# Performance work log

Hardware: AMD Instinct MI355X
Metric: run time of the kernel (lower is better)

The kernel has to match this reference:

```python
import jax, jax.numpy as jnp
import numpy as np

N_QUBITS = 14
DEPTH = 8
NUM_BLOCKS = DEPTH // 2
BATCH = 256
INIT_SCALE = 0.1


def _ry_mat(theta):
    # RY(t) = [[cos(t/2), -sin(t/2)], [sin(t/2), cos(t/2)]]; works for scalar or batched theta
    c = jnp.cos(theta / 2).astype(jnp.complex64)
    s = jnp.sin(theta / 2).astype(jnp.complex64)
    return jnp.stack([jnp.stack([c, -s], -1), jnp.stack([s, c], -1)], -2)


def _rz_mat(theta):
    # RZ(t) = diag(exp(-i t/2), exp(+i t/2))
    e = jnp.exp(-0.5j * theta.astype(jnp.complex64))
    z = jnp.zeros_like(e)
    return jnp.stack([jnp.stack([e, z], -1), jnp.stack([z, jnp.conj(e)], -1)], -2)


def _rx_mat(theta):
    # RX(t) = [[cos(t/2), -i sin(t/2)], [-i sin(t/2), cos(t/2)]] (target block of CRX)
    c = jnp.cos(theta / 2).astype(jnp.complex64)
    s = (-1j) * jnp.sin(theta / 2).astype(jnp.complex64)
    return jnp.stack([jnp.stack([c, s], -1), jnp.stack([s, c], -1)], -2)


def _apply_1q(state, mat, q, n):
    # state: (B, 2**n) complex64. Wire 0 = most significant axis (PennyLane convention).
    B = state.shape[0]
    s = state.reshape(B, 2 ** q, 2, 2 ** (n - q - 1))
    if mat.ndim == 3:  # per-sample angles (input encoding layer)
        out = jnp.einsum('bij,bljr->blir', mat, s)
    else:
        out = jnp.einsum('ij,bljr->blir', mat, s)
    return out.reshape(B, -1)


def _apply_ctrl(state, mat, c, t, n):
    # Apply 2x2 `mat` on target wire t where control wire c == 1.
    B = state.shape[0]
    s = state.reshape(B, 2 ** c, 2, 2 ** (n - c - 1))
    sub = s[:, :, 1, :]  # control = |1> subspace, (B, 2**c, 2**(n-c-1))
    p = t if t < c else t - 1  # target position in the reduced (n-1)-qubit register
    sub2 = sub.reshape(B, 2 ** p, 2, 2 ** (n - 2 - p))
    sub2 = jnp.einsum('ij,bljr->blir', mat, sub2)
    return s.at[:, :, 1, :].set(sub2.reshape(sub.shape)).reshape(B, -1)


def _circuit(inputs, weights):
    n, nb = N_QUBITS, NUM_BLOCKS
    B = inputs.shape[0]
    state = jnp.zeros((B, 2 ** n), jnp.complex64).at[:, 0].set(1.0)
    # input encoding: RY(inputs[..., q]) on each wire (batched angles)
    for q in range(n):
        state = _apply_1q(state, _ry_mat(inputs[:, q]), q, n)
    # weights flat index = b*3n + layer*n + q  ->  reshape (nb, 3, n)
    w = weights.reshape(nb, 3, n)
    X = jnp.asarray([[0, 1], [1, 0]], dtype=jnp.complex64)

    def block(st, wb):
        for q in range(n):
            st = _apply_1q(st, _ry_mat(wb[0, q]), q, n)
        for q in range(n):
            st = _apply_ctrl(st, X, q, (q + 1) % n, n)  # CNOT ring
        for q in range(n):
            st = _apply_1q(st, _rz_mat(wb[1, q]), q, n)
        for q in range(n):
            st = _apply_ctrl(st, _rx_mat(wb[2, q]), q, (q + 1) % n, n)  # CRX ring
        return st

    block = jax.checkpoint(block)
    for b in range(nb):
        state = block(state, w[b])

    # <Z_q> = P(bit_q = 0) - P(bit_q = 1)
    probs = state.real ** 2 + state.imag ** 2
    outs = []
    for q in range(n):
        pq = probs.reshape(B, 2 ** q, 2, -1)
        outs.append(pq[:, :, 0, :].sum((1, 2)) - pq[:, :, 1, :].sum((1, 2)))
    return jnp.stack(outs, -1).astype(jnp.float32)


def setup_inputs() -> dict:
    key = jax.random.key(0)
    k1, k2 = jax.random.split(key)
    inputs = jax.random.normal(k1, (BATCH, N_QUBITS), dtype=jnp.float32)
    weights = INIT_SCALE * jax.random.normal(k2, (3 * N_QUBITS * NUM_BLOCKS,), dtype=jnp.float32)
    return {"inputs": inputs, "weights": weights}


def reference(inputs, weights):
    return _circuit(inputs, weights)
```

## Files before the change

kernel.cpp:

```cpp
#include <hip/hip_runtime.h>
#include <utility>

#define NQ 14
#define NST (1 << NQ)
#define THREADS 1024

typedef float f2 __attribute__((ext_vector_type(2)));

struct PassD {
    unsigned short comboR[16];
    unsigned short rows[4];
    unsigned short tmask[4];
    unsigned short crx_widx[3];
    unsigned short ry_widx[3];
    unsigned char  ry_tb[3];
    unsigned char  ncrx;
    unsigned char  nry;
    short          rzidx;
    unsigned char  measfold;
};
struct RZD  { unsigned short rows_ng[10]; unsigned short widx_ng[10]; unsigned short widx_g[4]; };
struct AllD { PassD pass[20]; RZD rz[4]; unsigned short meas_rows_ng[10]; int npass; };

constexpr void fill_geom(PassD& P, const unsigned short* R, const unsigned short* C, const int* tb)
{
    for (int i = 0; i < 4; ++i) { P.tmask[i] = C[tb[i]]; P.rows[i] = R[tb[i]]; }
    for (int j = 0; j < 16; ++j) {
        unsigned short x = 0;
        for (int i = 0; i < 4; ++i) if ((j >> i) & 1) x = (unsigned short)(x ^ P.tmask[i]);
        P.comboR[j] = x;
    }
}

constexpr void ring(unsigned short* R, unsigned short* C) {
    for (int q = 0; q < NQ; ++q) {
        int cb = 13 - q, tb = 13 - ((q + 1) % NQ);
        R[tb] = (unsigned short)(R[tb] ^ R[cb]);
        C[cb] = (unsigned short)(C[cb] ^ C[tb]);
    }
}

constexpr AllD build_desc() {
    AllD A{};
    unsigned short R[NQ] = {}, C[NQ] = {};
    for (int k = 0; k < NQ; ++k) { R[k] = (unsigned short)(1u << k); C[k] = (unsigned short)(1u << k); }
    int np = 0;
    const int tiles[5][4] = {{13,12,11,10},{10,9,8,7},{7,6,5,4},{4,3,2,1},{1,0,13,2}};
    const int gfirst[5]   = {0, 3, 6, 9, 12};
    const int ngate[5]    = {3, 3, 3, 3, 2};
    const int rybits[5][3]= {{11,12,0},{10,9,8},{7,6,5},{4,3,2},{13,1,0}};
    const int nryp[5]     = {2, 3, 3, 3, 3};

    for (int blk = 0; blk < 4; ++blk) {
        ring(R, C);
        for (int pi = 0; pi < 5; ++pi) {
            PassD& P = A.pass[np];
            fill_geom(P, R, C, tiles[pi]);
            P.ncrx = (unsigned char)ngate[pi];
            for (int g = 0; g < 3; ++g)
                P.crx_widx[g] = (unsigned short)((g < ngate[pi]) ? blk*42 + 28 + gfirst[pi] + g : 0);
            if (blk < 3) {
                P.nry = (unsigned char)nryp[pi];
                for (int g = 0; g < 3; ++g) {
                    if (g < nryp[pi]) {
                        int k = rybits[pi][g];
                        P.ry_widx[g] = (unsigned short)((blk + 1)*42 + (13 - k));
                        int t = 0;
                        for (int i = 0; i < 4; ++i) if (tiles[pi][i] == k) t = i;
                        P.ry_tb[g] = (unsigned char)t;
                    } else { P.ry_widx[g] = 0; P.ry_tb[g] = 0; }
                }
            } else { P.nry = 0; for (int g = 0; g < 3; ++g) { P.ry_widx[g] = 0; P.ry_tb[g] = 0; } }
            P.rzidx = (short)((pi == 0) ? blk : -1);
            P.measfold = (unsigned char)((blk == 3 && pi == 4) ? 1 : 0);
            if (pi == 0) {
                RZD& Z = A.rz[blk];
                for (int i = 0; i < 4; ++i)
                    Z.widx_g[i] = (unsigned short)(blk*42 + 14 + (13 - tiles[0][i]));
                int t = 0;
                for (int q = 4; q < NQ; ++q, ++t) {
                    Z.rows_ng[t] = R[13 - q];
                    Z.widx_ng[t] = (unsigned short)(blk*42 + 14 + q);
                }
            }
            ++np;
        }
        if (blk == 3)
            for (int t = 0; t < 10; ++t) A.meas_rows_ng[t] = R[13 - (1 + t)];
    }
    A.npass = np;
    return A;
}

constexpr AllD A = build_desc();
static_assert(A.npass == 20, "expected 20 passes");

constexpr int parity14(unsigned v) { v ^= v >> 8; v ^= v >> 4; v ^= v >> 2; v ^= v >> 1; return (int)(v & 1); }

constexpr bool check_dual() {
    for (int p = 0; p < 20; ++p)
        for (int i = 0; i < 4; ++i)
            for (int j = 0; j < 4; ++j)
                if (parity14((unsigned)(A.pass[p].rows[i] & A.pass[p].tmask[j])) != (i == j ? 1 : 0))
                    return false;
    return true;
}
static_assert(check_dual(), "R/C duality violated");

struct GWT { unsigned short w[20][6]; };
constexpr GWT build_gwt() {
    GWT g{};
    for (int p = 0; p < 20; ++p) {
        for (int s = 0; s < 3; ++s) g.w[p][s]     = A.pass[p].crx_widx[s];
        for (int s = 0; s < 3; ++s) g.w[p][3 + s] = A.pass[p].ry_widx[s];
    }
    return g;
}
constexpr GWT GW = build_gwt();

constexpr int lead(unsigned short v) { int b = 13; while (b > 0 && !((v >> b) & 1)) --b; return b; }

struct Span {
    unsigned short red[14]; int n;
    constexpr unsigned short reduce(unsigned short v) const {
        for (int i = 0; i < n; ++i) { int lb = lead(red[i]); if ((v >> lb) & 1) v = (unsigned short)(v ^ red[i]); }
        return v;
    }
    constexpr bool add(unsigned short v) {
        unsigned short r = reduce(v);
        if (!r) return false;
        red[n++] = r; return true;
    }
};

constexpr unsigned short proj(unsigned short vec, const PassD& P) {
    unsigned short r = vec;
    for (int t = 0; t < 4; ++t)
        if (parity14((unsigned)(vec & P.rows[t]))) r = (unsigned short)(r ^ P.tmask[t]);
    return r;
}

struct VecsT { unsigned short lane[20][6]; unsigned short g[10][4]; int ok; };
constexpr VecsT build_vecs() {
    VecsT V{}; V.ok = 1;
    for (int k = 0; k < 10; ++k) {
        const PassD& P0 = A.pass[2*k];
        const PassD& P1 = A.pass[2*k + 1];
        Span SW{}; unsigned short Wb[10] = {}; int nw = 0;
        for (int i = 0; i < 4; ++i) if (SW.add(P0.tmask[i])) Wb[nw++] = P0.tmask[i];
        for (int i = 0; i < 4; ++i) if (nw < 10 && SW.add(P1.tmask[i])) Wb[nw++] = P1.tmask[i];
        for (int b = 0; b < 14 && nw < 10; ++b) {
            unsigned short e = (unsigned short)(1u << b);
            if (SW.add(e)) Wb[nw++] = e;
        }
        if (nw != 10) V.ok = 0;
        Span SG = SW; int ngv = 0;
        for (int b = 0; b < 14 && ngv < 4; ++b) {
            unsigned short e = (unsigned short)(1u << b);
            if (SG.add(e)) V.g[k][ngv++] = e;
        }
        if (ngv != 4) V.ok = 0;
        for (int pp = 0; pp < 2; ++pp) {
            const PassD& P = (pp == 0) ? P0 : P1;
            int pidx = 2*k + pp;
            Span ST{};
            for (int i = 0; i < 4; ++i) ST.add(P.tmask[i]);
            int nl = 0;
            for (int i = 0; i < 10 && nl < 6; ++i)
                if (ST.add(Wb[i])) V.lane[pidx][nl++] = Wb[i];
            if (nl != 6) V.ok = 0;
            Span SF{};
            for (int i = 0; i < 4; ++i) SF.add(P.tmask[i]);
            for (int i = 0; i < 6; ++i) if (!SF.add(V.lane[pidx][i])) V.ok = 0;
            for (int i = 0; i < 4; ++i) if (!SF.add(V.g[k][i])) V.ok = 0;
            if (SF.n != 14) V.ok = 0;
        }
    }
    return V;
}
constexpr VecsT VC = build_vecs();
static_assert(VC.ok == 1, "vec construction failed");

struct P6T { unsigned short u[20][6]; };
constexpr P6T build_p6() {
    P6T X{};
    for (int p = 0; p < 20; ++p)
        for (int i = 0; i < 6; ++i)
            X.u[p][i] = proj(VC.lane[p][i], A.pass[p]);
    return X;
}
constexpr P6T P6 = build_p6();

constexpr unsigned lmap(const unsigned short* row, unsigned x) {
    unsigned l = 0;
    for (int t = 0; t < 4; ++t) l |= (unsigned)parity14(row[t] & x) << t;
    return l;
}
constexpr int nib_rank(const unsigned* nibs, int n) {
    unsigned basis[4] = {};
    int r = 0;
    for (int i = 0; i < n; ++i) {
        unsigned v = nibs[i] & 15u;
        for (int b = 3; b >= 0 && v; --b) {
            if (!((v >> b) & 1)) continue;
            if (basis[b]) v ^= basis[b];
            else { basis[b] = v; ++r; v = 0; }
        }
    }
    return r;
}
struct Lp { unsigned short row[4]; int score; };

constexpr int full_score(const unsigned short* r) {
    unsigned cn[4] = {};
    for (int c = 0; c < 4; ++c) {
        unsigned v = 0;
        for (int t = 0; t < 4; ++t) v |= ((unsigned)(r[t] >> c) & 1u) << t;
        cn[c] = v;
    }
    if (nib_rank(cn, 4) != 4) return -1;
    int sc = 0;
    for (int p = 0; p < 20; ++p) {
        unsigned im[6] = {};
        for (int i = 0; i < 6; ++i) im[i] = lmap(r, P6.u[p][i]);
        if (nib_rank(im, 6) == 4) ++sc;
    }
    return sc;
}

constexpr Lp search_stage(unsigned seed, int iters) {
    Lp best{}; best.score = -1;
    unsigned s = seed;
    for (int it = 0; it < iters; ++it) {
        unsigned short r[4] = {};
        for (int t = 0; t < 4; ++t) { s = s*1664525u + 1013904223u; r[t] = (unsigned short)((s >> 9) & 0x3FFF); }
        unsigned cn[4] = {};
        for (int c = 0; c < 4; ++c) {
            unsigned v = 0;
            for (int t = 0; t < 4; ++t) v |= ((unsigned)(r[t] >> c) & 1u) << t;
            cn[c] = v;
        }
        if (nib_rank(cn, 4) != 4) continue;
        int sc = 0;
        for (int p = 0; p < 20; ++p) {
            unsigned im[6] = {};
            for (int i = 0; i < 6; ++i) im[i] = lmap(r, P6.u[p][i]);
            if (nib_rank(im, 6) != 4) break;
            ++sc;
        }
        if (sc > best.score) { best.score = sc; for (int t = 0; t < 4; ++t) best.row[t] = r[t]; }
        if (best.score == 20) break;
    }
    return best;
}
constexpr Lp S0 = search_stage(0x12345u, 500);
constexpr Lp S1 = search_stage(0xBEEF1u, 500);
constexpr Lp S2 = search_stage(0xC0FFEu, 500);
constexpr Lp S3 = search_stage(0x777A1u, 500);
constexpr Lp S4 = search_stage(0x51DE5u, 500);
constexpr Lp S5 = search_stage(0xA11CEu, 500);
constexpr Lp S6 = search_stage(0x0F00Du, 500);
constexpr Lp S7 = search_stage(0x9E3779u & 0xFFFFF, 500);
constexpr Lp S8 = search_stage(0x13579u, 500);
constexpr Lp S9 = search_stage(0x2468Au, 500);
constexpr Lp S10 = search_stage(0xFACE1u, 500);
constexpr Lp S11 = search_stage(0xD00D1u, 500);
constexpr Lp pick_best() {
    Lp b = S0;
    if (S1.score  > b.score) b = S1;
    if (S2.score  > b.score) b = S2;
    if (S3.score  > b.score) b = S3;
    if (S4.score  > b.score) b = S4;
    if (S5.score  > b.score) b = S5;
    if (S6.score  > b.score) b = S6;
    if (S7.score  > b.score) b = S7;
    if (S8.score  > b.score) b = S8;
    if (S9.score  > b.score) b = S9;
    if (S10.score > b.score) b = S10;
    if (S11.score > b.score) b = S11;
    return b;
}
constexpr Lp climb(Lp start, int sweeps) {
    Lp cur = start;
    for (int sw = 0; sw < sweeps && cur.score < 20; ++sw) {
        for (int t = 0; t < 4; ++t) {
            for (int b = 0; b < 14; ++b) {
                if (cur.score >= 20) break;
                unsigned short nr[4] = {cur.row[0], cur.row[1], cur.row[2], cur.row[3]};
                nr[t] = (unsigned short)(nr[t] ^ (1u << b));
                int sc = full_score(nr);
                if (sc > cur.score) { cur.score = sc; cur.row[t] = nr[t]; }
            }
        }
    }
    return cur;
}
constexpr Lp C0 = climb(pick_best(), 2);
constexpr Lp C1 = climb(C0, 2);
constexpr Lp LSEL = C1;
static_assert(LSEL.score >= 17, "bank-map search regressed");

constexpr unsigned short swz2(unsigned short x) {
    return (unsigned short)(((unsigned)x & ~15u) | lmap(LSEL.row, x));
}

constexpr int add_basis4(unsigned* basis, unsigned v) {
    for (int b = 3; b >= 0; --b) {
        if (!((v >> b) & 1)) continue;
        if (basis[b]) v ^= basis[b];
        else { basis[b] = v; return 1; }
    }
    return 0;
}
constexpr int add_basis6(unsigned* basis, unsigned v) {
    for (int b = 5; b >= 0; --b) {
        if (!((v >> b) & 1)) continue;
        if (basis[b]) v ^= basis[b];
        else { basis[b] = v; return 1; }
    }
    return 0;
}
struct LaneOrd { unsigned short lane[20][6]; };
constexpr LaneOrd build_lane2() {
    LaneOrd O{};
    for (int p = 0; p < 20; ++p) {
        for (int i = 0; i < 6; ++i) O.lane[p][i] = VC.lane[p][i];
        unsigned imu[6] = {};
        for (int i = 0; i < 6; ++i) imu[i] = lmap(LSEL.row, P6.u[p][i]);
        {
            unsigned chk[6] = {imu[0], imu[1], imu[2], imu[3], imu[4], imu[5]};
            if (nib_rank(chk, 6) != 4) continue;
        }
        unsigned short nl[6] = {};
        int ns = 0;
        unsigned ib[4] = {};
        unsigned sb[6] = {};
        for (unsigned c = 1; c < 64 && ns < 4; ++c) {
            unsigned img = 0; unsigned short rv = 0;
            for (int i = 0; i < 6; ++i) if ((c >> i) & 1) { img ^= imu[i]; rv = (unsigned short)(rv ^ VC.lane[p][i]); }
            if (img == 0) continue;
            unsigned ib2[4] = {ib[0], ib[1], ib[2], ib[3]};
            unsigned sb2[6] = {sb[0], sb[1], sb[2], sb[3], sb[4], sb[5]};
            if (add_basis4(ib2, img) && add_basis6(sb2, c)) {
                for (int t = 0; t < 4; ++t) ib[t] = ib2[t];
                for (int t = 0; t < 6; ++t) sb[t] = sb2[t];
                nl[ns++] = rv;
            }
        }
        for (unsigned c = 1; c < 64 && ns < 6; ++c) {
            unsigned img = 0; unsigned short rv = 0;
            for (int i = 0; i < 6; ++i) if ((c >> i) & 1) { img ^= imu[i]; rv = (unsigned short)(rv ^ VC.lane[p][i]); }
            if (img != 0) continue;
            unsigned sb2[6] = {sb[0], sb[1], sb[2], sb[3], sb[4], sb[5]};
            if (add_basis6(sb2, c)) {
                for (int t = 0; t < 6; ++t) sb[t] = sb2[t];
                nl[ns++] = rv;
            }
        }
        if (ns == 6)
            for (int i = 0; i < 6; ++i) O.lane[p][i] = nl[i];
    }
    return O;
}
constexpr LaneOrd LO = build_lane2();

struct CS2 { unsigned short c[20][16]; };
constexpr CS2 build_cs2() {
    CS2 C{};
    for (int p = 0; p < 20; ++p)
        for (int j = 0; j < 16; ++j)
            C.c[p][j] = swz2(A.pass[p].comboR[j]);
    return C;
}
constexpr CS2 CSS = build_cs2();

struct LJt { unsigned short v[16]; };
constexpr LJt build_lj() {
    LJt t{};
    for (int j = 0; j < 16; ++j) t.v[j] = (unsigned short)lmap(LSEL.row, (unsigned)(j * 1024));
    return t;
}
constexpr LJt LJ = build_lj();

constexpr unsigned pack_entry(unsigned short vec0, int p) {
    const PassD& P = A.pass[p];
    unsigned short vec = proj(vec0, P);
    unsigned par = 0;
    if (P.rzidx >= 0)
        for (int t = 0; t < 10; ++t) par |= (unsigned)parity14(vec & A.rz[P.rzidx].rows_ng[t]) << t;
    if (P.measfold)
        for (int t = 0; t < 10; ++t) par |= (unsigned)parity14(vec & A.meas_rows_ng[t]) << t;
    return ((unsigned)swz2(vec) << 3) | (par << 22);
}

struct LutsT { unsigned v[20][2][32]; };
constexpr LutsT build_luts() {
    LutsT L{};
    for (int p = 0; p < 20; ++p) {
        int k = p >> 1;
        for (int t = 0; t < 32; ++t) {
            unsigned short x = 0;
            for (int i = 0; i < 5; ++i) if ((t >> i) & 1) x = (unsigned short)(x ^ LO.lane[p][i]);
            L.v[p][0][t] = pack_entry(x, p);
            unsigned short y = 0;
            if (t & 1) y = (unsigned short)(y ^ LO.lane[p][5]);
            for (int i = 0; i < 4; ++i) if ((t >> (i + 1)) & 1) y = (unsigned short)(y ^ VC.g[k][i]);
            L.v[p][1][t] = pack_entry(y, p);
        }
    }
    return L;
}
constexpr LutsT LUTS = build_luts();
__device__ __constant__ LutsT cLUTS = LUTS;

template<int Pi>
__device__ __forceinline__ void run_pass(f2* st, const f2 (*tabG)[6], const float (*tabRZ)[14],
                                         unsigned comb, float* acc)
{
    constexpr PassD Pd = A.pass[Pi];
    char* stb = (char*)st;
    const int base = (int)(comb & 0x1FFF8u);
    const unsigned par = comb >> 22;

    f2 v[16];
#pragma unroll
    for (int j = 0; j < 16; ++j)
        v[j] = *(const f2*)(stb + (base ^ (CSS.c[Pi][j] << 3)));

    if constexpr (Pd.rzidx >= 0) {
        float phi0 = 0.f;
#pragma unroll
        for (int t = 0; t < 10; ++t) {
            float h = tabRZ[Pd.rzidx][t];
            phi0 += ((par >> t) & 1) ? h : -h;
        }
        const float h0 = tabRZ[Pd.rzidx][10], h1 = tabRZ[Pd.rzidx][11];
        const float h2 = tabRZ[Pd.rzidx][12], h3 = tabRZ[Pd.rzidx][13];
#pragma unroll
        for (int j = 0; j < 16; ++j) {
            float phi = ((((phi0 + ((j & 1) ? h0 : -h0)) + ((j & 2) ? h1 : -h1))
                                 + ((j & 4) ? h2 : -h2)) + ((j & 8) ? h3 : -h3));
            float s, c; __sincosf(phi, &s, &c);
            f2 C = {c, c}, S = {-s, s};
            v[j] = C * v[j] + S * v[j].yx;
        }
    }

#pragma unroll
    for (int g = 0; g < Pd.ncrx; ++g) {
        f2 cs = tabG[Pi][g];
        f2 C = {cs.x, cs.x}, S = {cs.y, -cs.y};
#pragma unroll
        for (int j = 0; j < 16; ++j) if (((j >> g) & 1) && !((j >> (g + 1)) & 1)) {
            int j1 = j | (1 << (g + 1));
            f2 a0 = v[j], a1 = v[j1];
            v[j]  = C * a0 + S * a1.yx;
            v[j1] = C * a1 + S * a0.yx;
        }
    }

#pragma unroll
    for (int g = 0; g < Pd.nry; ++g) {
        int t = Pd.ry_tb[g];
        f2 cs = tabG[Pi][3 + g];
        f2 C = {cs.x, cs.x}, Sv = {cs.y, cs.y}, NS = {-cs.y, -cs.y};
#pragma unroll
        for (int j = 0; j < 16; ++j) if (!((j >> t) & 1)) {
            int j1 = j | (1 << t);
            f2 a0 = v[j], a1 = v[j1];
            v[j]  = C * a0 + NS * a1;
            v[j1] = Sv * a0 + C * a1;
        }
    }

    if constexpr (Pd.measfold != 0) {
        f2 ps = {0.f, 0.f}, p0 = {0.f, 0.f}, p1 = {0.f, 0.f}, p2 = {0.f, 0.f}, p3 = {0.f, 0.f};
#pragma unroll
        for (int j = 0; j < 16; ++j) {
            f2 t2 = v[j] * v[j];
            ps += t2;
            if (j & 1) p0 += t2;
            if (j & 2) p1 += t2;
            if (j & 4) p2 += t2;
            if (j & 8) p3 += t2;
        }
        float psum = ps.x + ps.y;
        float pg0 = p0.x + p0.y, pg1 = p1.x + p1.y, pg2 = p2.x + p2.y, pg3 = p3.x + p3.y;
        acc[12] += psum - 2.f * pg0;
        acc[13] += psum - 2.f * pg1;
        acc[0]  += psum - 2.f * pg2;
        acc[11] += psum - 2.f * pg3;
#pragma unroll
        for (int t = 0; t < 10; ++t) {
            float sg = ((par >> t) & 1) ? -1.f : 1.f;
            acc[1 + t] += sg * psum;
        }
    } else {
#pragma unroll
        for (int j = 0; j < 16; ++j)
            *(f2*)(stb + (base ^ (CSS.c[Pi][j] << 3))) = v[j];
        if constexpr ((Pi & 1) != 0) __syncthreads();
    }
}

template<int... I>
__device__ __forceinline__ void run_all(std::integer_sequence<int, I...>,
                                        f2* st, const f2 (*tabG)[6], const float (*tabRZ)[14],
                                        const unsigned* comb, float* acc)
{
    (run_pass<I>(st, tabG, tabRZ, comb[I], acc), ...);
}

__global__ __launch_bounds__(THREADS, 4)
void qsim_kernel(const float* __restrict__ inputs,
                 const float* __restrict__ weights,
                 float* __restrict__ out)
{
    __shared__ f2     st[NST];
    __shared__ float  tab[256];
    __shared__ f2     tabG[20][6];
    __shared__ float  tabRZ[4][14];
    __shared__ float  red[THREADS / 64][NQ];

    const int b = blockIdx.x;
    const int tid = threadIdx.x;

    unsigned comb[20];
#pragma unroll
    for (int p = 0; p < 20; ++p)
        comb[p] = cLUTS.v[p][0][tid & 31] ^ cLUTS.v[p][1][tid >> 5];

    if (tid < 120) {
        int p = tid / 6, sl = tid - p * 6;
        float w = weights[GW.w[p][sl]];
        float s, c; __sincosf(0.5f * w, &s, &c);
        tabG[p][sl] = (f2){c, s};
    } else if (tid >= 128 && tid < 128 + 56) {
        int idx = tid - 128;
        int blk = idx / 14, k = idx - blk * 14;
        unsigned wi = (k < 10) ? A.rz[blk].widx_ng[k] : A.rz[blk].widx_g[k - 10];
        tabRZ[blk][k] = 0.5f * weights[wi];
    } else if (tid >= 256 && tid < 512) {
        int t = tid - 256;
        int half = t >> 7, tt = t & 127;
        float prod = 1.f;
#pragma unroll
        for (int j = 0; j < 7; ++j) {
            int xb = j + 7 * half;
            int q  = 13 - xb;
            float a = 0.5f * (inputs[b * NQ + q] + weights[q]);
            float s, c; __sincosf(a, &s, &c);
            prod *= ((tt >> j) & 1) ? s : c;
        }
        tab[t] = prod;
    }
    __syncthreads();

    unsigned l4t = 0;
#pragma unroll
    for (int t = 0; t < 4; ++t)
        l4t |= (unsigned)(__popc((int)(LSEL.row[t] & tid)) & 1) << t;
#pragma unroll
    for (int j = 0; j < 16; ++j) {
        int x = tid + j * THREADS;
        int addr = (x & ~15) | (int)(l4t ^ LJ.v[j]);
        st[addr] = (f2){tab[x & 127] * tab[128 + (x >> 7)], 0.f};
    }
    __syncthreads();

    float acc[NQ];
#pragma unroll
    for (int q = 0; q < NQ; ++q) acc[q] = 0.f;

    run_all(std::make_integer_sequence<int, 20>{}, st, tabG, tabRZ, comb, acc);

#pragma unroll
    for (int q = 0; q < NQ; ++q) {
        float v2 = acc[q];
        v2 += __shfl_down(v2, 32);
        v2 += __shfl_down(v2, 16);
        v2 += __shfl_down(v2, 8);
        v2 += __shfl_down(v2, 4);
        v2 += __shfl_down(v2, 2);
        v2 += __shfl_down(v2, 1);
        acc[q] = v2;
    }
    const int wave = tid >> 6, lane = tid & 63;
    if (lane == 0) {
#pragma unroll
        for (int q = 0; q < NQ; ++q) red[wave][q] = acc[q];
    }
    __syncthreads();
    if (tid < NQ) {
        float v2 = 0.f;
#pragma unroll
        for (int w = 0; w < THREADS / 64; ++w) v2 += red[w][tid];
        out[b * NQ + tid] = v2;
    }
}

extern "C" void kernel_launch(void* const* d_in, const int* in_sizes, int n_in,
                              void* d_out, int out_size, void* d_ws, size_t ws_size,
                              hipStream_t stream) {
    const float* inputs  = (const float*)d_in[0];
    const float* weights = (const float*)d_in[1];
    float* out = (float*)d_out;
    const int B = in_sizes[0] / NQ;
    qsim_kernel<<<dim3(B), dim3(THREADS), 0, stream>>>(inputs, weights, out);
}
```

Baseline: 46.47 us.

## Use 5-qubit tiles with 512 threads to cut passes from 20 to 16

Enlarges each register-resident tile from 4 to 5 qubits, so each thread holds 32 amplitudes instead of 16. The block shrinks to 512 threads and the gate schedule is regrouped into 4 passes per block instead of 5. This cuts shared-memory round trips and barriers. The costs are higher register pressure, lower occupancy per block, and a weaker bank-conflict map score (the assert is relaxed to at least 13 of 16 passes), so there may be more LDS bank conflicts.

```diff
diff --git a/kernel.cpp b/kernel.cpp
--- a/kernel.cpp
+++ b/kernel.cpp
@@ -3,31 +3,33 @@
 
 #define NQ 14
 #define NST (1 << NQ)
-#define THREADS 1024
+#define THREADS 512
+#define NP 16
+#define NE 32
 
 typedef float f2 __attribute__((ext_vector_type(2)));
 
 struct PassD {
-    unsigned short comboR[16];
-    unsigned short rows[4];
-    unsigned short tmask[4];
-    unsigned short crx_widx[3];
-    unsigned short ry_widx[3];
-    unsigned char  ry_tb[3];
+    unsigned short comboR[NE];
+    unsigned short rows[5];
+    unsigned short tmask[5];
+    unsigned short crx_widx[4];
+    unsigned short ry_widx[4];
+    unsigned char  ry_tb[4];
     unsigned char  ncrx;
     unsigned char  nry;
     short          rzidx;
     unsigned char  measfold;
 };
-struct RZD  { unsigned short rows_ng[10]; unsigned short widx_ng[10]; unsigned short widx_g[4]; };
-struct AllD { PassD pass[20]; RZD rz[4]; unsigned short meas_rows_ng[10]; int npass; };
+struct RZD  { unsigned short rows_ng[9]; unsigned short widx_ng[9]; unsigned short widx_g[5]; };
+struct AllD { PassD pass[NP]; RZD rz[4]; unsigned short meas_rows_ng[9]; int npass; };
 
 constexpr void fill_geom(PassD& P, const unsigned short* R, const unsigned short* C, const int* tb)
 {
-    for (int i = 0; i < 4; ++i) { P.tmask[i] = C[tb[i]]; P.rows[i] = R[tb[i]]; }
-    for (int j = 0; j < 16; ++j) {
+    for (int i = 0; i < 5; ++i) { P.tmask[i] = C[tb[i]]; P.rows[i] = R[tb[i]]; }
+    for (int j = 0; j < NE; ++j) {
         unsigned short x = 0;
-        for (int i = 0; i < 4; ++i) if ((j >> i) & 1) x = (unsigned short)(x ^ P.tmask[i]);
+        for (int i = 0; i < 5; ++i) if ((j >> i) & 1) x = (unsigned short)(x ^ P.tmask[i]);
         P.comboR[j] = x;
     }
 }
@@ -45,40 +47,40 @@
     unsigned short R[NQ] = {}, C[NQ] = {};
     for (int k = 0; k < NQ; ++k) { R[k] = (unsigned short)(1u << k); C[k] = (unsigned short)(1u << k); }
     int np = 0;
-    const int tiles[5][4] = {{13,12,11,10},{10,9,8,7},{7,6,5,4},{4,3,2,1},{1,0,13,2}};
-    const int gfirst[5]   = {0, 3, 6, 9, 12};
-    const int ngate[5]    = {3, 3, 3, 3, 2};
-    const int rybits[5][3]= {{11,12,0},{10,9,8},{7,6,5},{4,3,2},{13,1,0}};
-    const int nryp[5]     = {2, 3, 3, 3, 3};
+    const int tiles[4][5]  = {{13,12,11,10,9},{9,8,7,6,5},{5,4,3,2,1},{1,0,13,3,2}};
+    const int gfirst[4]    = {0, 4, 8, 12};
+    const int ngate[4]     = {4, 4, 4, 2};
+    const int rybits[4][4] = {{12,11,10,0},{9,8,7,6},{5,4,3,2},{13,1,0,0}};
+    const int nryp[4]      = {3, 4, 4, 3};
 
     for (int blk = 0; blk < 4; ++blk) {
         ring(R, C);
-        for (int pi = 0; pi < 5; ++pi) {
+        for (int pi = 0; pi < 4; ++pi) {
             PassD& P = A.pass[np];
             fill_geom(P, R, C, tiles[pi]);
             P.ncrx = (unsigned char)ngate[pi];
-            for (int g = 0; g < 3; ++g)
+            for (int g = 0; g < 4; ++g)
                 P.crx_widx[g] = (unsigned short)((g < ngate[pi]) ? blk*42 + 28 + gfirst[pi] + g : 0);
             if (blk < 3) {
                 P.nry = (unsigned char)nryp[pi];
-                for (int g = 0; g < 3; ++g) {
+                for (int g = 0; g < 4; ++g) {
                     if (g < nryp[pi]) {
                         int k = rybits[pi][g];
                         P.ry_widx[g] = (unsigned short)((blk + 1)*42 + (13 - k));
                         int t = 0;
-                        for (int i = 0; i < 4; ++i) if (tiles[pi][i] == k) t = i;
+                        for (int i = 0; i < 5; ++i) if (tiles[pi][i] == k) t = i;
                         P.ry_tb[g] = (unsigned char)t;
                     } else { P.ry_widx[g] = 0; P.ry_tb[g] = 0; }
                 }
-            } else { P.nry = 0; for (int g = 0; g < 3; ++g) { P.ry_widx[g] = 0; P.ry_tb[g] = 0; } }
+            } else { P.nry = 0; for (int g = 0; g < 4; ++g) { P.ry_widx[g] = 0; P.ry_tb[g] = 0; } }
             P.rzidx = (short)((pi == 0) ? blk : -1);
-            P.measfold = (unsigned char)((blk == 3 && pi == 4) ? 1 : 0);
+            P.measfold = (unsigned char)((blk == 3 && pi == 3) ? 1 : 0);
             if (pi == 0) {
                 RZD& Z = A.rz[blk];
-                for (int i = 0; i < 4; ++i)
+                for (int i = 0; i < 5; ++i)
                     Z.widx_g[i] = (unsigned short)(blk*42 + 14 + (13 - tiles[0][i]));
                 int t = 0;
-                for (int q = 4; q < NQ; ++q, ++t) {
+                for (int q = 5; q < NQ; ++q, ++t) {
                     Z.rows_ng[t] = R[13 - q];
                     Z.widx_ng[t] = (unsigned short)(blk*42 + 14 + q);
                 }
@@ -86,33 +88,33 @@
             ++np;
         }
         if (blk == 3)
-            for (int t = 0; t < 10; ++t) A.meas_rows_ng[t] = R[13 - (1 + t)];
+            for (int t = 0; t < 9; ++t) A.meas_rows_ng[t] = R[13 - (1 + t)];
     }
     A.npass = np;
     return A;
 }
 
 constexpr AllD A = build_desc();
-static_assert(A.npass == 20, "expected 20 passes");
+static_assert(A.npass == NP, "expected 16 passes");
 
 constexpr int parity14(unsigned v) { v ^= v >> 8; v ^= v >> 4; v ^= v >> 2; v ^= v >> 1; return (int)(v & 1); }
 
 constexpr bool check_dual() {
-    for (int p = 0; p < 20; ++p)
-        for (int i = 0; i < 4; ++i)
-            for (int j = 0; j < 4; ++j)
+    for (int p = 0; p < NP; ++p)
+        for (int i = 0; i < 5; ++i)
+            for (int j = 0; j < 5; ++j)
                 if (parity14((unsigned)(A.pass[p].rows[i] & A.pass[p].tmask[j])) != (i == j ? 1 : 0))
                     return false;
     return true;
 }
 static_assert(check_dual(), "R/C duality violated");
 
-struct GWT { unsigned short w[20][6]; };
+struct GWT { unsigned short w[NP][8]; };
 constexpr GWT build_gwt() {
     GWT g{};
-    for (int p = 0; p < 20; ++p) {
-        for (int s = 0; s < 3; ++s) g.w[p][s]     = A.pass[p].crx_widx[s];
-        for (int s = 0; s < 3; ++s) g.w[p][3 + s] = A.pass[p].ry_widx[s];
+    for (int p = 0; p < NP; ++p) {
+        for (int s = 0; s < 4; ++s) g.w[p][s]     = A.pass[p].crx_widx[s];
+        for (int s = 0; s < 4; ++s) g.w[p][4 + s] = A.pass[p].ry_widx[s];
     }
     return g;
 }
@@ -135,44 +137,44 @@
 
 constexpr unsigned short proj(unsigned short vec, const PassD& P) {
     unsigned short r = vec;
-    for (int t = 0; t < 4; ++t)
+    for (int t = 0; t < 5; ++t)
         if (parity14((unsigned)(vec & P.rows[t]))) r = (unsigned short)(r ^ P.tmask[t]);
     return r;
 }
 
-struct VecsT { unsigned short lane[20][6]; unsigned short g[10][4]; int ok; };
+struct VecsT { unsigned short lane[NP][6]; unsigned short g[NP/2][3]; int ok; };
 constexpr VecsT build_vecs() {
     VecsT V{}; V.ok = 1;
-    for (int k = 0; k < 10; ++k) {
+    for (int k = 0; k < NP/2; ++k) {
         const PassD& P0 = A.pass[2*k];
         const PassD& P1 = A.pass[2*k + 1];
-        Span SW{}; unsigned short Wb[10] = {}; int nw = 0;
-        for (int i = 0; i < 4; ++i) if (SW.add(P0.tmask[i])) Wb[nw++] = P0.tmask[i];
-        for (int i = 0; i < 4; ++i) if (nw < 10 && SW.add(P1.tmask[i])) Wb[nw++] = P1.tmask[i];
-        for (int b = 0; b < 14 && nw < 10; ++b) {
+        Span SW{}; unsigned short Wb[11] = {}; int nw = 0;
+        for (int i = 0; i < 5; ++i) if (SW.add(P0.tmask[i])) Wb[nw++] = P0.tmask[i];
+        for (int i = 0; i < 5; ++i) if (nw < 11 && SW.add(P1.tmask[i])) Wb[nw++] = P1.tmask[i];
+        for (int b = 0; b < 14 && nw < 11; ++b) {
             unsigned short e = (unsigned short)(1u << b);
             if (SW.add(e)) Wb[nw++] = e;
         }
-        if (nw != 10) V.ok = 0;
+        if (nw != 11) V.ok = 0;
         Span SG = SW; int ngv = 0;
-        for (int b = 0; b < 14 && ngv < 4; ++b) {
+        for (int b = 0; b < 14 && ngv < 3; ++b) {
             unsigned short e = (unsigned short)(1u << b);
             if (SG.add(e)) V.g[k][ngv++] = e;
         }
-        if (ngv != 4) V.ok = 0;
+        if (ngv != 3) V.ok = 0;
         for (int pp = 0; pp < 2; ++pp) {
             const PassD& P = (pp == 0) ? P0 : P1;
             int pidx = 2*k + pp;
             Span ST{};
-            for (int i = 0; i < 4; ++i) ST.add(P.tmask[i]);
+            for (int i = 0; i < 5; ++i) ST.add(P.tmask[i]);
             int nl = 0;
-            for (int i = 0; i < 10 && nl < 6; ++i)
+            for (int i = 0; i < 11 && nl < 6; ++i)
                 if (ST.add(Wb[i])) V.lane[pidx][nl++] = Wb[i];
             if (nl != 6) V.ok = 0;
             Span SF{};
-            for (int i = 0; i < 4; ++i) SF.add(P.tmask[i]);
+            for (int i = 0; i < 5; ++i) SF.add(P.tmask[i]);
             for (int i = 0; i < 6; ++i) if (!SF.add(V.lane[pidx][i])) V.ok = 0;
-            for (int i = 0; i < 4; ++i) if (!SF.add(V.g[k][i])) V.ok = 0;
+            for (int i = 0; i < 3; ++i) if (!SF.add(V.g[k][i])) V.ok = 0;
             if (SF.n != 14) V.ok = 0;
         }
     }
@@ -181,10 +183,10 @@
 constexpr VecsT VC = build_vecs();
 static_assert(VC.ok == 1, "vec construction failed");
 
-struct P6T { unsigned short u[20][6]; };
+struct P6T { unsigned short u[NP][6]; };
 constexpr P6T build_p6() {
     P6T X{};
-    for (int p = 0; p < 20; ++p)
+    for (int p = 0; p < NP; ++p)
         for (int i = 0; i < 6; ++i)
             X.u[p][i] = proj(VC.lane[p][i], A.pass[p]);
     return X;
@@ -220,7 +222,7 @@
     }
     if (nib_rank(cn, 4) != 4) return -1;
     int sc = 0;
-    for (int p = 0; p < 20; ++p) {
+    for (int p = 0; p < NP; ++p) {
         unsigned im[6] = {};
         for (int i = 0; i < 6; ++i) im[i] = lmap(r, P6.u[p][i]);
         if (nib_rank(im, 6) == 4) ++sc;
@@ -234,58 +236,37 @@
     for (int it = 0; it < iters; ++it) {
         unsigned short r[4] = {};
         for (int t = 0; t < 4; ++t) { s = s*1664525u + 1013904223u; r[t] = (unsigned short)((s >> 9) & 0x3FFF); }
-        unsigned cn[4] = {};
-        for (int c = 0; c < 4; ++c) {
-            unsigned v = 0;
-            for (int t = 0; t < 4; ++t) v |= ((unsigned)(r[t] >> c) & 1u) << t;
-            cn[c] = v;
-        }
-        if (nib_rank(cn, 4) != 4) continue;
-        int sc = 0;
-        for (int p = 0; p < 20; ++p) {
-            unsigned im[6] = {};
-            for (int i = 0; i < 6; ++i) im[i] = lmap(r, P6.u[p][i]);
-            if (nib_rank(im, 6) != 4) break;
-            ++sc;
-        }
+        int sc = full_score(r);
         if (sc > best.score) { best.score = sc; for (int t = 0; t < 4; ++t) best.row[t] = r[t]; }
-        if (best.score == 20) break;
+        if (best.score == NP) break;
     }
     return best;
 }
-constexpr Lp S0 = search_stage(0x12345u, 500);
-constexpr Lp S1 = search_stage(0xBEEF1u, 500);
-constexpr Lp S2 = search_stage(0xC0FFEu, 500);
-constexpr Lp S3 = search_stage(0x777A1u, 500);
-constexpr Lp S4 = search_stage(0x51DE5u, 500);
-constexpr Lp S5 = search_stage(0xA11CEu, 500);
-constexpr Lp S6 = search_stage(0x0F00Du, 500);
-constexpr Lp S7 = search_stage(0x9E3779u & 0xFFFFF, 500);
-constexpr Lp S8 = search_stage(0x13579u, 500);
-constexpr Lp S9 = search_stage(0x2468Au, 500);
-constexpr Lp S10 = search_stage(0xFACE1u, 500);
-constexpr Lp S11 = search_stage(0xD00D1u, 500);
+constexpr Lp S0 = search_stage(0x12345u, 400);
+constexpr Lp S1 = search_stage(0xBEEF1u, 400);
+constexpr Lp S2 = search_stage(0xC0FFEu, 400);
+constexpr Lp S3 = search_stage(0x777A1u, 400);
+constexpr Lp S4 = search_stage(0x51DE5u, 400);
+constexpr Lp S5 = search_stage(0xA11CEu, 400);
+constexpr Lp S6 = search_stage(0x0F00Du, 400);
+constexpr Lp S7 = search_stage(0x13579u, 400);
 constexpr Lp pick_best() {
     Lp b = S0;
-    if (S1.score  > b.score) b = S1;
-    if (S2.score  > b.score) b = S2;
-    if (S3.score  > b.score) b = S3;
-    if (S4.score  > b.score) b = S4;
-    if (S5.score  > b.score) b = S5;
-    if (S6.score  > b.score) b = S6;
-    if (S7.score  > b.score) b = S7;
-    if (S8.score  > b.score) b = S8;
-    if (S9.score  > b.score) b = S9;
-    if (S10.score > b.score) b = S10;
-    if (S11.score > b.score) b = S11;
+    if (S1.score > b.score) b = S1;
+    if (S2.score > b.score) b = S2;
+    if (S3.score > b.score) b = S3;
+    if (S4.score > b.score) b = S4;
+    if (S5.score > b.score) b = S5;
+    if (S6.score > b.score) b = S6;
+    if (S7.score > b.score) b = S7;
     return b;
 }
 constexpr Lp climb(Lp start, int sweeps) {
     Lp cur = start;
-    for (int sw = 0; sw < sweeps && cur.score < 20; ++sw) {
+    for (int sw = 0; sw < sweeps && cur.score < NP; ++sw) {
         for (int t = 0; t < 4; ++t) {
             for (int b = 0; b < 14; ++b) {
-                if (cur.score >= 20) break;
+                if (cur.score >= NP) break;
                 unsigned short nr[4] = {cur.row[0], cur.row[1], cur.row[2], cur.row[3]};
                 nr[t] = (unsigned short)(nr[t] ^ (1u << b));
                 int sc = full_score(nr);
@@ -298,7 +279,7 @@
 constexpr Lp C0 = climb(pick_best(), 2);
 constexpr Lp C1 = climb(C0, 2);
 constexpr Lp LSEL = C1;
-static_assert(LSEL.score >= 17, "bank-map search regressed");
+static_assert(LSEL.score >= 13, "bank-map search failed badly");
 
 constexpr unsigned short swz2(unsigned short x) {
     return (unsigned short)(((unsigned)x & ~15u) | lmap(LSEL.row, x));
@@ -320,10 +301,10 @@
     }
     return 0;
 }
-struct LaneOrd { unsigned short lane[20][6]; };
+struct LaneOrd { unsigned short lane[NP][6]; };
 constexpr LaneOrd build_lane2() {
     LaneOrd O{};
-    for (int p = 0; p < 20; ++p) {
+    for (int p = 0; p < NP; ++p) {
         for (int i = 0; i < 6; ++i) O.lane[p][i] = VC.lane[p][i];
         unsigned imu[6] = {};
         for (int i = 0; i < 6; ++i) imu[i] = lmap(LSEL.row, P6.u[p][i]);
@@ -364,20 +345,20 @@
 }
 constexpr LaneOrd LO = build_lane2();
 
-struct CS2 { unsigned short c[20][16]; };
+struct CS2 { unsigned short c[NP][NE]; };
 constexpr CS2 build_cs2() {
     CS2 C{};
-    for (int p = 0; p < 20; ++p)
-        for (int j = 0; j < 16; ++j)
+    for (int p = 0; p < NP; ++p)
+        for (int j = 0; j < NE; ++j)
             C.c[p][j] = swz2(A.pass[p].comboR[j]);
     return C;
 }
 constexpr CS2 CSS = build_cs2();
 
-struct LJt { unsigned short v[16]; };
+struct LJt { unsigned short v[NE]; };
 constexpr LJt build_lj() {
     LJt t{};
-    for (int j = 0; j < 16; ++j) t.v[j] = (unsigned short)lmap(LSEL.row, (unsigned)(j * 1024));
+    for (int j = 0; j < NE; ++j) t.v[j] = (unsigned short)lmap(LSEL.row, (unsigned)(j * THREADS));
     return t;
 }
 constexpr LJt LJ = build_lj();
@@ -387,24 +368,26 @@
     unsigned short vec = proj(vec0, P);
     unsigned par = 0;
     if (P.rzidx >= 0)
-        for (int t = 0; t < 10; ++t) par |= (unsigned)parity14(vec & A.rz[P.rzidx].rows_ng[t]) << t;
+        for (int t = 0; t < 9; ++t) par |= (unsigned)parity14(vec & A.rz[P.rzidx].rows_ng[t]) << t;
     if (P.measfold)
-        for (int t = 0; t < 10; ++t) par |= (unsigned)parity14(vec & A.meas_rows_ng[t]) << t;
+        for (int t = 0; t < 9; ++t) par |= (unsigned)parity14(vec & A.meas_rows_ng[t]) << t;
     return ((unsigned)swz2(vec) << 3) | (par << 22);
 }
 
-struct LutsT { unsigned v[20][2][32]; };
+struct LutsT { unsigned v[NP][2][32]; };
 constexpr LutsT build_luts() {
     LutsT L{};
-    for (int p = 0; p < 20; ++p) {
+    for (int p = 0; p < NP; ++p) {
         int k = p >> 1;
         for (int t = 0; t < 32; ++t) {
             unsigned short x = 0;
             for (int i = 0; i < 5; ++i) if ((t >> i) & 1) x = (unsigned short)(x ^ LO.lane[p][i]);
             L.v[p][0][t] = pack_entry(x, p);
+        }
+        for (int t = 0; t < 16; ++t) {
             unsigned short y = 0;
             if (t & 1) y = (unsigned short)(y ^ LO.lane[p][5]);
-            for (int i = 0; i < 4; ++i) if ((t >> (i + 1)) & 1) y = (unsigned short)(y ^ VC.g[k][i]);
+            for (int i = 0; i < 3; ++i) if ((t >> (i + 1)) & 1) y = (unsigned short)(y ^ VC.g[k][i]);
             L.v[p][1][t] = pack_entry(y, p);
         }
     }
@@ -414,7 +397,7 @@
 __device__ __constant__ LutsT cLUTS = LUTS;
 
 template<int Pi>
-__device__ __forceinline__ void run_pass(f2* st, const f2 (*tabG)[6], const float (*tabRZ)[14],
+__device__ __forceinline__ void run_pass(f2* st, const f2 (*tabG)[8], const float (*tabRZ)[14],
                                          unsigned comb, float* acc)
 {
     constexpr PassD Pd = A.pass[Pi];
@@ -422,24 +405,26 @@
     const int base = (int)(comb & 0x1FFF8u);
     const unsigned par = comb >> 22;
 
-    f2 v[16];
-#pragma unroll
-    for (int j = 0; j < 16; ++j)
+    f2 v[NE];
+#pragma unroll
+    for (int j = 0; j < NE; ++j)
         v[j] = *(const f2*)(stb + (base ^ (CSS.c[Pi][j] << 3)));
 
     if constexpr (Pd.rzidx >= 0) {
         float phi0 = 0.f;
 #pragma unroll
-        for (int t = 0; t < 10; ++t) {
+        for (int t = 0; t < 9; ++t) {
             float h = tabRZ[Pd.rzidx][t];
             phi0 += ((par >> t) & 1) ? h : -h;
         }
-        const float h0 = tabRZ[Pd.rzidx][10], h1 = tabRZ[Pd.rzidx][11];
-        const float h2 = tabRZ[Pd.rzidx][12], h3 = tabRZ[Pd.rzidx][13];
-#pragma unroll
-        for (int j = 0; j < 16; ++j) {
-            float phi = ((((phi0 + ((j & 1) ? h0 : -h0)) + ((j & 2) ? h1 : -h1))
-                                 + ((j & 4) ? h2 : -h2)) + ((j & 8) ? h3 : -h3));
+        const float h0 = tabRZ[Pd.rzidx][9],  h1 = tabRZ[Pd.rzidx][10];
+        const float h2 = tabRZ[Pd.rzidx][11], h3 = tabRZ[Pd.rzidx][12];
+        const float h4 = tabRZ[Pd.rzidx][13];
+#pragma unroll
+        for (int j = 0; j < NE; ++j) {
+            float phi = (((((phi0 + ((j & 1) ? h0 : -h0)) + ((j & 2) ? h1 : -h1))
+                                  + ((j & 4) ? h2 : -h2)) + ((j & 8) ? h3 : -h3))
+                                  + ((j & 16) ? h4 : -h4));
             float s, c; __sincosf(phi, &s, &c);
             f2 C = {c, c}, S = {-s, s};
             v[j] = C * v[j] + S * v[j].yx;
@@ -451,7 +436,7 @@
         f2 cs = tabG[Pi][g];
         f2 C = {cs.x, cs.x}, S = {cs.y, -cs.y};
 #pragma unroll
-        for (int j = 0; j < 16; ++j) if (((j >> g) & 1) && !((j >> (g + 1)) & 1)) {
+        for (int j = 0; j < NE; ++j) if (((j >> g) & 1) && !((j >> (g + 1)) & 1)) {
             int j1 = j | (1 << (g + 1));
             f2 a0 = v[j], a1 = v[j1];
             v[j]  = C * a0 + S * a1.yx;
@@ -462,10 +447,10 @@
 #pragma unroll
     for (int g = 0; g < Pd.nry; ++g) {
         int t = Pd.ry_tb[g];
-        f2 cs = tabG[Pi][3 + g];
+        f2 cs = tabG[Pi][4 + g];
         f2 C = {cs.x, cs.x}, Sv = {cs.y, cs.y}, NS = {-cs.y, -cs.y};
 #pragma unroll
-        for (int j = 0; j < 16; ++j) if (!((j >> t) & 1)) {
+        for (int j = 0; j < NE; ++j) if (!((j >> t) & 1)) {
             int j1 = j | (1 << t);
             f2 a0 = v[j], a1 = v[j1];
             v[j]  = C * a0 + NS * a1;
@@ -474,30 +459,33 @@
     }
 
     if constexpr (Pd.measfold != 0) {
-        f2 ps = {0.f, 0.f}, p0 = {0.f, 0.f}, p1 = {0.f, 0.f}, p2 = {0.f, 0.f}, p3 = {0.f, 0.f};
-#pragma unroll
-        for (int j = 0; j < 16; ++j) {
+        f2 ps = {0.f, 0.f}, p0 = {0.f, 0.f}, p1 = {0.f, 0.f}, p2 = {0.f, 0.f}, p3 = {0.f, 0.f}, p4 = {0.f, 0.f};
+#pragma unroll
+        for (int j = 0; j < NE; ++j) {
             f2 t2 = v[j] * v[j];
             ps += t2;
-            if (j & 1) p0 += t2;
-            if (j & 2) p1 += t2;
-            if (j & 4) p2 += t2;
-            if (j & 8) p3 += t2;
+            if (j & 1)  p0 += t2;
+            if (j & 2)  p1 += t2;
+            if (j & 4)  p2 += t2;
+            if (j & 8)  p3 += t2;
+            if (j & 16) p4 += t2;
         }
         float psum = ps.x + ps.y;
-        float pg0 = p0.x + p0.y, pg1 = p1.x + p1.y, pg2 = p2.x + p2.y, pg3 = p3.x + p3.y;
+        float pg0 = p0.x + p0.y, pg1 = p1.x + p1.y, pg2 = p2.x + p2.y;
+        float pg3 = p3.x + p3.y, pg4 = p4.x + p4.y;
         acc[12] += psum - 2.f * pg0;
         acc[13] += psum - 2.f * pg1;
         acc[0]  += psum - 2.f * pg2;
-        acc[11] += psum - 2.f * pg3;
-#pragma unroll
-        for (int t = 0; t < 10; ++t) {
+        acc[10] += psum - 2.f * pg3;
+        acc[11] += psum - 2.f * pg4;
+#pragma unroll
+        for (int t = 0; t < 9; ++t) {
             float sg = ((par >> t) & 1) ? -1.f : 1.f;
             acc[1 + t] += sg * psum;
         }
     } else {
 #pragma unroll
-        for (int j = 0; j < 16; ++j)
+        for (int j = 0; j < NE; ++j)
             *(f2*)(stb + (base ^ (CSS.c[Pi][j] << 3))) = v[j];
         if constexpr ((Pi & 1) != 0) __syncthreads();
     }
@@ -505,42 +493,42 @@
 
 template<int... I>
 __device__ __forceinline__ void run_all(std::integer_sequence<int, I...>,
-                                        f2* st, const f2 (*tabG)[6], const float (*tabRZ)[14],
+                                        f2* st, const f2 (*tabG)[8], const float (*tabRZ)[14],
                                         const unsigned* comb, float* acc)
 {
     (run_pass<I>(st, tabG, tabRZ, comb[I], acc), ...);
 }
 
-__global__ __launch_bounds__(THREADS, 4)
+__global__ __launch_bounds__(THREADS, 2)
 void qsim_kernel(const float* __restrict__ inputs,
                  const float* __restrict__ weights,
                  float* __restrict__ out)
 {
     __shared__ f2     st[NST];
     __shared__ float  tab[256];
-    __shared__ f2     tabG[20][6];
+    __shared__ f2     tabG[NP][8];
     __shared__ float  tabRZ[4][14];
     __shared__ float  red[THREADS / 64][NQ];
 
     const int b = blockIdx.x;
     const int tid = threadIdx.x;
 
-    unsigned comb[20];
-#pragma unroll
-    for (int p = 0; p < 20; ++p)
+    unsigned comb[NP];
+#pragma unroll
+    for (int p = 0; p < NP; ++p)
         comb[p] = cLUTS.v[p][0][tid & 31] ^ cLUTS.v[p][1][tid >> 5];
 
-    if (tid < 120) {
-        int p = tid / 6, sl = tid - p * 6;
+    if (tid < 128) {
+        int p = tid >> 3, sl = tid & 7;
         float w = weights[GW.w[p][sl]];
         float s, c; __sincosf(0.5f * w, &s, &c);
         tabG[p][sl] = (f2){c, s};
     } else if (tid >= 128 && tid < 128 + 56) {
         int idx = tid - 128;
         int blk = idx / 14, k = idx - blk * 14;
-        unsigned wi = (k < 10) ? A.rz[blk].widx_ng[k] : A.rz[blk].widx_g[k - 10];
+        unsigned wi = (k < 9) ? A.rz[blk].widx_ng[k] : A.rz[blk].widx_g[k - 9];
         tabRZ[blk][k] = 0.5f * weights[wi];
-    } else if (tid >= 256 && tid < 512) {
+    } else if (tid >= 256) {
         int t = tid - 256;
         int half = t >> 7, tt = t & 127;
         float prod = 1.f;
@@ -561,7 +549,7 @@
     for (int t = 0; t < 4; ++t)
         l4t |= (unsigned)(__popc((int)(LSEL.row[t] & tid)) & 1) << t;
 #pragma unroll
-    for (int j = 0; j < 16; ++j) {
+    for (int j = 0; j < NE; ++j) {
         int x = tid + j * THREADS;
         int addr = (x & ~15) | (int)(l4t ^ LJ.v[j]);
         st[addr] = (f2){tab[x & 127] * tab[128 + (x >> 7)], 0.f};
@@ -572,7 +560,7 @@
 #pragma unroll
     for (int q = 0; q < NQ; ++q) acc[q] = 0.f;
 
-    run_all(std::make_integer_sequence<int, 20>{}, st, tabG, tabRZ, comb, acc);
+    run_all(std::make_integer_sequence<int, NP>{}, st, tabG, tabRZ, comb, acc);
 
 #pragma unroll
     for (int q = 0; q < NQ; ++q) {
```

New measurement: 42.97 us (median of 2 runs). 7.5% less time.
